# Kernel tuning notes

Measured on AMD Instinct MI355X. Metric: run time of the kernel, lower is better.

Reference implementation:

```python
import jax, jax.numpy as jnp
import numpy as np

B, T, D, U, C = 256, 512, 128, 128, 64


def setup_inputs() -> dict:
    key = jax.random.key(0)
    ks = jax.random.split(key, 4)
    s_in = 1.0 / np.sqrt(D)
    s_u = 1.0 / np.sqrt(U)
    return {
        "inputs": jax.random.normal(ks[0], (B, T, D), dtype=jnp.float32),
        "W1": jax.random.normal(ks[1], (D, U), dtype=jnp.float32) * s_in,
        "b1": jnp.zeros((U,), dtype=jnp.float32),
        "W2": jax.random.normal(ks[2], (U, U), dtype=jnp.float32) * s_u,
        "b2": jnp.zeros((U,), dtype=jnp.float32),
        "Wc": jax.random.normal(ks[3], (U, C), dtype=jnp.float32) * s_u,
        "bc": jnp.zeros((C,), dtype=jnp.float32),
    }


def reference(inputs, W1, b1, W2, b2, Wc, bc):
    # state_{t} = tanh(x_t @ W1 + b1) + tanh(state_{t-1} @ W2 + b2)
    # Input projection has no recurrent dependency -> precompute in one big GEMM.
    h = jnp.tanh(jnp.einsum("btd,du->btu", inputs, W1) + b1)  # (B, T, U)

    def step(state, h_t):
        y = h_t + jnp.tanh(state @ W2 + b2)  # (B, U)
        return y, y

    state0 = jnp.zeros((inputs.shape[0], W2.shape[0]), dtype=inputs.dtype)
    _, ys = jax.lax.scan(step, state0, jnp.swapaxes(h, 0, 1))  # ys: (T, B, U)
    features = jnp.swapaxes(ys, 0, 1)  # (B, T, U)
    # classifier: Dense head applied to stacked features
    return jnp.einsum("btu,uc->btc", features, Wc) + bc
```

## Files before the change

### kernel.cpp

```cpp
#include <hip/hip_runtime.h>

#define NB 256
#define NT 512
#define ND 128
#define NU 128
#define NC 64
#define NM (NB * NT)
#define YP 136
#define SCL 2.8853900817779268f

typedef _Float16 half2v __attribute__((ext_vector_type(2)));
typedef _Float16 half4v __attribute__((ext_vector_type(4)));
typedef _Float16 half8v __attribute__((ext_vector_type(8)));
typedef float f32x4 __attribute__((ext_vector_type(4)));
typedef float v2f __attribute__((ext_vector_type(2)));

#define MFMA(a, b, c) __builtin_amdgcn_mfma_f32_16x16x32_f16((a), (b), (c), 0, 0, 0)

__device__ __forceinline__ half2v pk2(float a, float b) {
  return __builtin_bit_cast(half2v, __builtin_amdgcn_cvt_pkrtz(a, b));
}

__device__ __forceinline__ float tanh_s(float s) {
  float e = __builtin_amdgcn_exp2f(s);
  return fmaf(-2.0f, __builtin_amdgcn_rcpf(e + 1.0f), 1.0f);
}
__device__ __forceinline__ float ym1(float s, float th) {
  float e = __builtin_amdgcn_exp2f(s);
  return fmaf(-2.0f, __builtin_amdgcn_rcpf(e + 1.0f), th);
}

__device__ __forceinline__ void wg_barrier() {
  asm volatile("s_waitcnt lgkmcnt(0)\n\ts_barrier" ::: "memory");
}

__global__ __launch_bounds__(256, 1) void k1_inproj(
    const float* __restrict__ x, const float* __restrict__ W1,
    const float* __restrict__ b1v, _Float16* __restrict__ TH)
{
  __shared__ _Float16 W1T[ND * YP];
  const int tid = (int)threadIdx.x;
  for (int i = tid; i < ND * NU / 2; i += 256) {
    int n = i & 127, kh = i >> 7;
    half2v p = {(_Float16)(SCL * W1[(size_t)(2 * kh) * NU + n]),
                (_Float16)(SCL * W1[(size_t)(2 * kh + 1) * NU + n])};
    *(half2v*)&W1T[n * YP + 2 * kh] = p;
  }
  __syncthreads();

  const int L = tid & 63, wv = tid >> 6;
  const int v = L & 15, q = L >> 4;
  const int m0 = (int)blockIdx.x * 64 + wv * 16;

  const float* xr = x + (size_t)(m0 + v) * ND + 8 * q;
  half8v xf[4];
#pragma unroll
  for (int kk = 0; kk < 4; ++kk) {
    float4 a = *(const float4*)(xr + 32 * kk);
    float4 b = *(const float4*)(xr + 32 * kk + 4);
    half2v p0 = pk2(a.x, a.y), p1 = pk2(a.z, a.w);
    half2v p2 = pk2(b.x, b.y), p3 = pk2(b.z, b.w);
    xf[kk] = (half8v){p0[0], p0[1], p1[0], p1[1], p2[0], p2[1], p3[0], p3[1]};
  }

#pragma unroll
  for (int ht = 0; ht < 8; ++ht) {
    f32x4 acc;
    {
      float4 bb = *(const float4*)&b1v[16 * ht + 4 * q];
      acc = (f32x4){SCL * bb.x, SCL * bb.y, SCL * bb.z, SCL * bb.w};
    }
#pragma unroll
    for (int kk = 0; kk < 4; ++kk) {
      half8v wa = *(const half8v*)&W1T[(16 * ht + v) * YP + 32 * kk + 8 * q];
      acc = MFMA(wa, xf[kk], acc);
    }
    half2v zlo = pk2(tanh_s(acc[0]), tanh_s(acc[1]));
    half2v zhi = pk2(tanh_s(acc[2]), tanh_s(acc[3]));
    half4v z = {zlo[0], zlo[1], zhi[0], zhi[1]};
    *(half4v*)&TH[(size_t)(m0 + v) * NU + 16 * ht + 4 * q] = z;
  }
}

__global__ __launch_bounds__(640, 1) void k2_recur(
    const _Float16* __restrict__ TH, const float* __restrict__ W2,
    const float* __restrict__ b2v, const float* __restrict__ Wc,
    const float* __restrict__ bcv, float* __restrict__ out)
{
  __shared__ _Float16 Ybuf[2][2048];

  const int tid = (int)threadIdx.x;
  const int w = tid >> 6;
  const int L = tid & 63;
  const int v = L & 15, q = L >> 4;
  const int b0 = (int)blockIdx.x * 16;
  const _Float16* rd = &Ybuf[0][0] + L * 8;
  const f32x4 zero4 = (f32x4){0.f, 0.f, 0.f, 0.f};

  if (w < 8) {
    half8v w2f[4];
#pragma unroll
    for (int kk = 0; kk < 4; ++kk) {
      half8v h;
#pragma unroll
      for (int j = 0; j < 8; ++j)
        h[j] = (_Float16)(SCL * W2[(size_t)(32 * kk + 8 * q + j) * NU + 16 * w + v]);
      w2f[kk] = h;
    }
    f32x4 racc, b2f;
    {
      const int h0 = 16 * w + 4 * q;
      float4 bb = *(const float4*)&b2v[h0];
      racc = (f32x4){SCL * bb.x, SCL * bb.y, SCL * bb.z, SCL * bb.w};
      f32x4 cs = zero4;
#pragma unroll 4
      for (int k = 0; k < NU; ++k) {
        float4 ww = *(const float4*)&W2[(size_t)k * NU + h0];
        cs += (f32x4){ww.x, ww.y, ww.z, ww.w};
      }
      b2f = racc + (f32x4){SCL * cs[0], SCL * cs[1], SCL * cs[2], SCL * cs[3]};
    }

    const _Float16* thp = TH + ((size_t)(b0 + v) * NT) * NU + 16 * w + 4 * q;
    _Float16* wr = &Ybuf[0][0] + (w >> 1) * 512 +
                   (v + 16 * (2 * (w & 1) + (q >> 1))) * 8 + 4 * (q & 1);

    half4v thr0 = *(const half4v*)(thp + 0 * NU);
    half4v thr1 = *(const half4v*)(thp + 1 * NU);
    half4v thr2 = *(const half4v*)(thp + 2 * NU);
    half4v thr3 = *(const half4v*)(thp + 3 * NU);

    __builtin_amdgcn_s_setprio(1);

#define RSTEP(T_, THR_, BUF_)                                                 \
  {                                                                           \
    half2v ylo = pk2(ym1(racc[0], (float)THR_[0]),                            \
                     ym1(racc[1], (float)THR_[1]));                           \
    half2v yhi = pk2(ym1(racc[2], (float)THR_[2]),                            \
                     ym1(racc[3], (float)THR_[3]));                           \
    half4v y4 = {ylo[0], ylo[1], yhi[0], yhi[1]};                             \
    *(half4v*)(wr + (BUF_) * 2048) = y4;                                      \
    {                                                                         \
      int tn = (T_) + 4; tn = tn < NT ? tn : NT - 1;                          \
      THR_ = *(const half4v*)(thp + (size_t)tn * NU);                         \
    }                                                                         \
    wg_barrier();                                                             \
    {                                                                         \
      half8v yf0 = *(const half8v*)(rd + (BUF_) * 2048 + 0);                  \
      half8v yf1 = *(const half8v*)(rd + (BUF_) * 2048 + 512);                \
      half8v yf2 = *(const half8v*)(rd + (BUF_) * 2048 + 1024);               \
      half8v yf3 = *(const half8v*)(rd + (BUF_) * 2048 + 1536);               \
      f32x4 ra = MFMA(w2f[0], yf0, b2f);        \
      f32x4 rb = MFMA(w2f[1], yf1, zero4);                                    \
      ra = MFMA(w2f[2], yf2, ra);                                             \
      rb = MFMA(w2f[3], yf3, rb);                                             \
      racc = ra + rb;                                                         \
    }                                                                         \
  }

#pragma unroll 1
    for (int t = 0; t < NT; t += 4) {
      RSTEP(t + 0, thr0, 0)
      RSTEP(t + 1, thr1, 1)
      RSTEP(t + 2, thr2, 0)
      RSTEP(t + 3, thr3, 1)
    }
#undef RSTEP
  } else {
    const int hw = w - 8;
    half8v wcf[2][4];
    f32x4 bcf[2];
#pragma unroll
    for (int c2 = 0; c2 < 2; ++c2) {
      const int ct = 2 * hw + c2;
#pragma unroll
      for (int kk = 0; kk < 4; ++kk) {
        half8v h;
#pragma unroll
        for (int j = 0; j < 8; ++j)
          h[j] = (_Float16)Wc[(size_t)(32 * kk + 8 * q + j) * NC + 16 * ct + v];
        wcf[c2][kk] = h;
      }
      const int c0 = 16 * ct + 4 * q;
      float4 bb = *(const float4*)&bcv[c0];
      f32x4 cs = zero4;
#pragma unroll 4
      for (int k = 0; k < NU; ++k) {
        float4 ww = *(const float4*)&Wc[(size_t)k * NC + c0];
        cs += (f32x4){ww.x, ww.y, ww.z, ww.w};
      }
      bcf[c2] = cs + (f32x4){bb.x, bb.y, bb.z, bb.w};
    }
    float* op = out + ((size_t)(b0 + v) * NT) * NC + 4 * q + 32 * hw;

    half8v pf0, pf1, pf2, pf3;
#pragma unroll 1
    for (int t = 0; t < NT; ++t) {
      wg_barrier();
      if (t > 0) {
#pragma unroll
        for (int c2 = 0; c2 < 2; ++c2) {
          f32x4 oa = MFMA(wcf[c2][0], pf0, bcf[c2]);
          f32x4 ob = MFMA(wcf[c2][1], pf1, zero4);
          oa = MFMA(wcf[c2][2], pf2, oa);
          ob = MFMA(wcf[c2][3], pf3, ob);
          f32x4 oo = oa + ob;
          *(float4*)(op + (size_t)(t - 1) * NC + 16 * c2) =
              (float4){oo[0], oo[1], oo[2], oo[3]};
        }
      }
      const _Float16* rb = rd + (t & 1) * 2048;
      pf0 = *(const half8v*)(rb + 0);
      pf1 = *(const half8v*)(rb + 512);
      pf2 = *(const half8v*)(rb + 1024);
      pf3 = *(const half8v*)(rb + 1536);
    }
    asm volatile("s_waitcnt lgkmcnt(0)" ::: "memory");
#pragma unroll
    for (int c2 = 0; c2 < 2; ++c2) {
      f32x4 oa = MFMA(wcf[c2][0], pf0, bcf[c2]);
      f32x4 ob = MFMA(wcf[c2][1], pf1, zero4);
      oa = MFMA(wcf[c2][2], pf2, oa);
      ob = MFMA(wcf[c2][3], pf3, ob);
      f32x4 oo = oa + ob;
      *(float4*)(op + (size_t)(NT - 1) * NC + 16 * c2) =
          (float4){oo[0], oo[1], oo[2], oo[3]};
    }
  }
}

__device__ __forceinline__ float fast_tanh(float x) {
  float e = __expf(2.0f * x);
  return 1.0f - 2.0f / (e + 1.0f);
}
__device__ __forceinline__ float bcast(float val, int i) {
  return __builtin_bit_cast(float, __builtin_amdgcn_readlane(__builtin_bit_cast(int, val), i));
}

__global__ __launch_bounds__(256, 1) void rnn_fallback(
    const float* __restrict__ x, const float* __restrict__ W1,
    const float* __restrict__ b1v, const float* __restrict__ W2,
    const float* __restrict__ b2v, const float* __restrict__ Wc,
    const float* __restrict__ bcv, float* __restrict__ out)
{
  __shared__ float xring[16][ND];
  __shared__ float pH[2][4][NU];
  __shared__ float pR[2][4][NU];
  __shared__ float pC[2][4][NC];

  const int tid  = (int)threadIdx.x;
  const int lane = tid & 63;
  const int kg   = tid >> 6;
  const int b    = (int)blockIdx.x;
  const float4* xr4 = (const float4*)(x + (size_t)b * NT * ND);

  v2f w1f[32], w2f[32];
  float wcf[32];
#pragma unroll
  for (int i = 0; i < 32; ++i) {
    int k = kg * 32 + i;
    w1f[i] = (v2f){W1[k * NU + lane], W1[k * NU + lane + 64]};
    w2f[i] = (v2f){W2[k * NU + lane], W2[k * NU + lane + 64]};
    wcf[i] = Wc[k * NC + lane];
  }
  const float biasc = bcv[lane];
  float bias1 = 0.f, bias2 = 0.f;
  if (lane < 32) { bias1 = b1v[kg * 32 + lane]; bias2 = b2v[kg * 32 + lane]; }

  float4 stg = make_float4(0.f, 0.f, 0.f, 0.f);
  if (lane < 32) {
    float4 a0 = xr4[(kg + 0) * 32 + lane];
    float4 a1 = xr4[(kg + 4) * 32 + lane];
    ((float4*)xring[kg + 0])[lane] = a0;
    ((float4*)xring[kg + 4])[lane] = a1;
    stg = xr4[(kg + 8) * 32 + lane];
  }
  float yseg = 0.f;
  wg_barrier();

  for (int t = 0; t < NT; ++t) {
    const int pb = t & 1;
    v2f accH0 = {0.f, 0.f}, accH1 = {0.f, 0.f};
    const float4* xb = (const float4*)&xring[t & 15][kg * 32];
#pragma unroll
    for (int i = 0; i < 4; ++i) {
      float4 xa = xb[2 * i];
      float4 xc = xb[2 * i + 1];
      accH0 = w1f[8*i+0] * (v2f){xa.x, xa.x} + accH0;
      accH1 = w1f[8*i+1] * (v2f){xa.y, xa.y} + accH1;
      accH0 = w1f[8*i+2] * (v2f){xa.z, xa.z} + accH0;
      accH1 = w1f[8*i+3] * (v2f){xa.w, xa.w} + accH1;
      accH0 = w1f[8*i+4] * (v2f){xc.x, xc.x} + accH0;
      accH1 = w1f[8*i+5] * (v2f){xc.y, xc.y} + accH1;
      accH0 = w1f[8*i+6] * (v2f){xc.z, xc.z} + accH0;
      accH1 = w1f[8*i+7] * (v2f){xc.w, xc.w} + accH1;
    }
    v2f accH = accH0 + accH1;
    v2f accR0 = {0.f, 0.f}, accR1 = {0.f, 0.f};
    float accC0 = 0.f, accC1 = 0.f;
#pragma unroll
    for (int i = 0; i < 16; ++i) {
      float s0 = bcast(yseg, 2 * i);
      float s1 = bcast(yseg, 2 * i + 1);
      accR0 = w2f[2*i+0] * (v2f){s0, s0} + accR0;
      accR1 = w2f[2*i+1] * (v2f){s1, s1} + accR1;
      accC0 = fmaf(s0, wcf[2*i+0], accC0);
      accC1 = fmaf(s1, wcf[2*i+1], accC1);
    }
    v2f accR = accR0 + accR1;
    float accC = accC0 + accC1;

    pH[pb][kg][lane]      = accH.x;
    pH[pb][kg][lane + 64] = accH.y;
    pR[pb][kg][lane]      = accR.x;
    pR[pb][kg][lane + 64] = accR.y;
    pC[pb][kg][lane]      = accC;

    if (kg == (t & 3)) {
      if (lane < 32) {
        ((float4*)xring[(t + 8) & 15])[lane] = stg;
        int r = t + 12; r = (r < NT) ? r : (NT - 1);
        stg = xr4[r * 32 + lane];
      }
    }
    wg_barrier();
    if (lane < 32) {
      const int j = kg * 32 + lane;
      float hs = bias1, rs = bias2;
#pragma unroll
      for (int g = 0; g < 4; ++g) { hs += pH[pb][g][j]; rs += pR[pb][g][j]; }
      yseg = fast_tanh(hs) + fast_tanh(rs);
    }
    if (kg == ((t + 2) & 3) && t >= 1) {
      float cs = biasc;
#pragma unroll
      for (int g = 0; g < 4; ++g) cs += pC[pb][g][lane];
      out[((size_t)b * NT + (t - 1)) * NC + lane] = cs;
    }
  }
  float accC0 = 0.f, accC1 = 0.f;
#pragma unroll
  for (int i = 0; i < 16; ++i) {
    float s0 = bcast(yseg, 2 * i);
    float s1 = bcast(yseg, 2 * i + 1);
    accC0 = fmaf(s0, wcf[2*i+0], accC0);
    accC1 = fmaf(s1, wcf[2*i+1], accC1);
  }
  pC[0][kg][lane] = accC0 + accC1;
  wg_barrier();
  if (kg == 0) {
    float cs = biasc;
#pragma unroll
    for (int g = 0; g < 4; ++g) cs += pC[0][g][lane];
    out[((size_t)b * NT + (NT - 1)) * NC + lane] = cs;
  }
}

extern "C" void kernel_launch(void* const* d_in, const int* in_sizes, int n_in,
                              void* d_out, int out_size, void* d_ws, size_t ws_size,
                              hipStream_t stream) {
  (void)in_sizes; (void)n_in; (void)out_size;
  const float* x   = (const float*)d_in[0];
  const float* W1  = (const float*)d_in[1];
  const float* b1v = (const float*)d_in[2];
  const float* W2  = (const float*)d_in[3];
  const float* b2v = (const float*)d_in[4];
  const float* Wc  = (const float*)d_in[5];
  const float* bcv = (const float*)d_in[6];
  float* out = (float*)d_out;

  const size_t need = (size_t)NM * NU * 2;
  if (ws_size >= need) {
    _Float16* TH = (_Float16*)d_ws;
    hipLaunchKernelGGL(k1_inproj, dim3(NM / 64), dim3(256), 0, stream, x, W1, b1v, TH);
    hipLaunchKernelGGL(k2_recur, dim3(NB / 16), dim3(640), 0, stream,
                       TH, W2, b2v, Wc, bcv, out);
  } else {
    hipLaunchKernelGGL(rnn_fallback, dim3(NB), dim3(256), 0, stream,
                       x, W1, b1v, W2, b2v, Wc, bcv, out);
  }
}
```

Baseline: 302.3 us.

## Fuse input projection into recurrent kernel via producer warps and LDS ring

Removes the separate input-projection kernel and its fp16 global workspace. Four extra producer waves per block compute tanh(x W1 + b1) a few timesteps ahead into an 8-slot LDS ring that the recurrent waves read each step. This drops the global round trip for TH and one kernel launch. In exchange the 16 blocks now also carry the projection GEMM, the block grows to 896 threads, and the producers join every barrier on the serial critical path. The fallback kernel is deleted.

```diff
diff --git a/kernel.cpp b/kernel.cpp
--- a/kernel.cpp
+++ b/kernel.cpp
@@ -5,15 +5,12 @@
 #define ND 128
 #define NU 128
 #define NC 64
-#define NM (NB * NT)
-#define YP 136
 #define SCL 2.8853900817779268f
 
 typedef _Float16 half2v __attribute__((ext_vector_type(2)));
 typedef _Float16 half4v __attribute__((ext_vector_type(4)));
 typedef _Float16 half8v __attribute__((ext_vector_type(8)));
 typedef float f32x4 __attribute__((ext_vector_type(4)));
-typedef float v2f __attribute__((ext_vector_type(2)));
 
 #define MFMA(a, b, c) __builtin_amdgcn_mfma_f32_16x16x32_f16((a), (b), (c), 0, 0, 0)
 
@@ -34,60 +31,14 @@
   asm volatile("s_waitcnt lgkmcnt(0)\n\ts_barrier" ::: "memory");
 }
 
-__global__ __launch_bounds__(256, 1) void k1_inproj(
+__global__ __launch_bounds__(896, 1) void rnn_fused(
     const float* __restrict__ x, const float* __restrict__ W1,
-    const float* __restrict__ b1v, _Float16* __restrict__ TH)
-{
-  __shared__ _Float16 W1T[ND * YP];
-  const int tid = (int)threadIdx.x;
-  for (int i = tid; i < ND * NU / 2; i += 256) {
-    int n = i & 127, kh = i >> 7;
-    half2v p = {(_Float16)(SCL * W1[(size_t)(2 * kh) * NU + n]),
-                (_Float16)(SCL * W1[(size_t)(2 * kh + 1) * NU + n])};
-    *(half2v*)&W1T[n * YP + 2 * kh] = p;
-  }
-  __syncthreads();
-
-  const int L = tid & 63, wv = tid >> 6;
-  const int v = L & 15, q = L >> 4;
-  const int m0 = (int)blockIdx.x * 64 + wv * 16;
-
-  const float* xr = x + (size_t)(m0 + v) * ND + 8 * q;
-  half8v xf[4];
-#pragma unroll
-  for (int kk = 0; kk < 4; ++kk) {
-    float4 a = *(const float4*)(xr + 32 * kk);
-    float4 b = *(const float4*)(xr + 32 * kk + 4);
-    half2v p0 = pk2(a.x, a.y), p1 = pk2(a.z, a.w);
-    half2v p2 = pk2(b.x, b.y), p3 = pk2(b.z, b.w);
-    xf[kk] = (half8v){p0[0], p0[1], p1[0], p1[1], p2[0], p2[1], p3[0], p3[1]};
-  }
-
-#pragma unroll
-  for (int ht = 0; ht < 8; ++ht) {
-    f32x4 acc;
-    {
-      float4 bb = *(const float4*)&b1v[16 * ht + 4 * q];
-      acc = (f32x4){SCL * bb.x, SCL * bb.y, SCL * bb.z, SCL * bb.w};
-    }
-#pragma unroll
-    for (int kk = 0; kk < 4; ++kk) {
-      half8v wa = *(const half8v*)&W1T[(16 * ht + v) * YP + 32 * kk + 8 * q];
-      acc = MFMA(wa, xf[kk], acc);
-    }
-    half2v zlo = pk2(tanh_s(acc[0]), tanh_s(acc[1]));
-    half2v zhi = pk2(tanh_s(acc[2]), tanh_s(acc[3]));
-    half4v z = {zlo[0], zlo[1], zhi[0], zhi[1]};
-    *(half4v*)&TH[(size_t)(m0 + v) * NU + 16 * ht + 4 * q] = z;
-  }
-}
-
-__global__ __launch_bounds__(640, 1) void k2_recur(
-    const _Float16* __restrict__ TH, const float* __restrict__ W2,
+    const float* __restrict__ b1v, const float* __restrict__ W2,
     const float* __restrict__ b2v, const float* __restrict__ Wc,
     const float* __restrict__ bcv, float* __restrict__ out)
 {
   __shared__ _Float16 Ybuf[2][2048];
+  __shared__ _Float16 TR[8][2048];
 
   const int tid = (int)threadIdx.x;
   const int w = tid >> 6;
@@ -120,36 +71,30 @@
       }
       b2f = racc + (f32x4){SCL * cs[0], SCL * cs[1], SCL * cs[2], SCL * cs[3]};
     }
-
-    const _Float16* thp = TH + ((size_t)(b0 + v) * NT) * NU + 16 * w + 4 * q;
     _Float16* wr = &Ybuf[0][0] + (w >> 1) * 512 +
                    (v + 16 * (2 * (w & 1) + (q >> 1))) * 8 + 4 * (q & 1);
-
-    half4v thr0 = *(const half4v*)(thp + 0 * NU);
-    half4v thr1 = *(const half4v*)(thp + 1 * NU);
-    half4v thr2 = *(const half4v*)(thp + 2 * NU);
-    half4v thr3 = *(const half4v*)(thp + 3 * NU);
+    const _Float16* trr = &TR[0][0] + w * 256 + v * 16 + q * 4;
 
     __builtin_amdgcn_s_setprio(1);
-
-#define RSTEP(T_, THR_, BUF_)                                                 \
+    wg_barrier();
+
+    half4v thr = *(const half4v*)trr;
+
+#define RSTEP(T_, BUF_)                                                       \
   {                                                                           \
-    half2v ylo = pk2(ym1(racc[0], (float)THR_[0]),                            \
-                     ym1(racc[1], (float)THR_[1]));                           \
-    half2v yhi = pk2(ym1(racc[2], (float)THR_[2]),                            \
-                     ym1(racc[3], (float)THR_[3]));                           \
+    half2v ylo = pk2(ym1(racc[0], (float)thr[0]),                             \
+                     ym1(racc[1], (float)thr[1]));                            \
+    half2v yhi = pk2(ym1(racc[2], (float)thr[2]),                             \
+                     ym1(racc[3], (float)thr[3]));                            \
     half4v y4 = {ylo[0], ylo[1], yhi[0], yhi[1]};                             \
     *(half4v*)(wr + (BUF_) * 2048) = y4;                                      \
-    {                                                                         \
-      int tn = (T_) + 4; tn = tn < NT ? tn : NT - 1;                          \
-      THR_ = *(const half4v*)(thp + (size_t)tn * NU);                         \
-    }                                                                         \
     wg_barrier();                                                             \
     {                                                                         \
       half8v yf0 = *(const half8v*)(rd + (BUF_) * 2048 + 0);                  \
       half8v yf1 = *(const half8v*)(rd + (BUF_) * 2048 + 512);                \
       half8v yf2 = *(const half8v*)(rd + (BUF_) * 2048 + 1024);               \
       half8v yf3 = *(const half8v*)(rd + (BUF_) * 2048 + 1536);               \
+      thr = *(const half4v*)(trr + (((T_) + 1) & 7) * 2048);                  \
       f32x4 ra = MFMA(w2f[0], yf0, b2f);        \
       f32x4 rb = MFMA(w2f[1], yf1, zero4);                                    \
       ra = MFMA(w2f[2], yf2, ra);                                             \
@@ -159,14 +104,13 @@
   }
 
 #pragma unroll 1
-    for (int t = 0; t < NT; t += 4) {
-      RSTEP(t + 0, thr0, 0)
-      RSTEP(t + 1, thr1, 1)
-      RSTEP(t + 2, thr2, 0)
-      RSTEP(t + 3, thr3, 1)
+    for (int t = 0; t < NT; t += 2) {
+      RSTEP(t + 0, 0)
+      RSTEP(t + 1, 1)
     }
 #undef RSTEP
-  } else {
+
+  } else if (w < 10) {
     const int hw = w - 8;
     half8v wcf[2][4];
     f32x4 bcf[2];
@@ -192,6 +136,8 @@
       bcf[c2] = cs + (f32x4){bb.x, bb.y, bb.z, bb.w};
     }
     float* op = out + ((size_t)(b0 + v) * NT) * NC + 4 * q + 32 * hw;
+
+    wg_barrier();
 
     half8v pf0, pf1, pf2, pf3;
 #pragma unroll 1
@@ -226,140 +172,86 @@
       *(float4*)(op + (size_t)(NT - 1) * NC + 16 * c2) =
           (float4){oo[0], oo[1], oo[2], oo[3]};
     }
-  }
-}
-
-__device__ __forceinline__ float fast_tanh(float x) {
-  float e = __expf(2.0f * x);
-  return 1.0f - 2.0f / (e + 1.0f);
-}
-__device__ __forceinline__ float bcast(float val, int i) {
-  return __builtin_bit_cast(float, __builtin_amdgcn_readlane(__builtin_bit_cast(int, val), i));
-}
-
-__global__ __launch_bounds__(256, 1) void rnn_fallback(
-    const float* __restrict__ x, const float* __restrict__ W1,
-    const float* __restrict__ b1v, const float* __restrict__ W2,
-    const float* __restrict__ b2v, const float* __restrict__ Wc,
-    const float* __restrict__ bcv, float* __restrict__ out)
-{
-  __shared__ float xring[16][ND];
-  __shared__ float pH[2][4][NU];
-  __shared__ float pR[2][4][NU];
-  __shared__ float pC[2][4][NC];
-
-  const int tid  = (int)threadIdx.x;
-  const int lane = tid & 63;
-  const int kg   = tid >> 6;
-  const int b    = (int)blockIdx.x;
-  const float4* xr4 = (const float4*)(x + (size_t)b * NT * ND);
-
-  v2f w1f[32], w2f[32];
-  float wcf[32];
-#pragma unroll
-  for (int i = 0; i < 32; ++i) {
-    int k = kg * 32 + i;
-    w1f[i] = (v2f){W1[k * NU + lane], W1[k * NU + lane + 64]};
-    w2f[i] = (v2f){W2[k * NU + lane], W2[k * NU + lane + 64]};
-    wcf[i] = Wc[k * NC + lane];
-  }
-  const float biasc = bcv[lane];
-  float bias1 = 0.f, bias2 = 0.f;
-  if (lane < 32) { bias1 = b1v[kg * 32 + lane]; bias2 = b2v[kg * 32 + lane]; }
-
-  float4 stg = make_float4(0.f, 0.f, 0.f, 0.f);
-  if (lane < 32) {
-    float4 a0 = xr4[(kg + 0) * 32 + lane];
-    float4 a1 = xr4[(kg + 4) * 32 + lane];
-    ((float4*)xring[kg + 0])[lane] = a0;
-    ((float4*)xring[kg + 4])[lane] = a1;
-    stg = xr4[(kg + 8) * 32 + lane];
-  }
-  float yseg = 0.f;
-  wg_barrier();
-
-  for (int t = 0; t < NT; ++t) {
-    const int pb = t & 1;
-    v2f accH0 = {0.f, 0.f}, accH1 = {0.f, 0.f};
-    const float4* xb = (const float4*)&xring[t & 15][kg * 32];
-#pragma unroll
-    for (int i = 0; i < 4; ++i) {
-      float4 xa = xb[2 * i];
-      float4 xc = xb[2 * i + 1];
-      accH0 = w1f[8*i+0] * (v2f){xa.x, xa.x} + accH0;
-      accH1 = w1f[8*i+1] * (v2f){xa.y, xa.y} + accH1;
-      accH0 = w1f[8*i+2] * (v2f){xa.z, xa.z} + accH0;
-      accH1 = w1f[8*i+3] * (v2f){xa.w, xa.w} + accH1;
-      accH0 = w1f[8*i+4] * (v2f){xc.x, xc.x} + accH0;
-      accH1 = w1f[8*i+5] * (v2f){xc.y, xc.y} + accH1;
-      accH0 = w1f[8*i+6] * (v2f){xc.z, xc.z} + accH0;
-      accH1 = w1f[8*i+7] * (v2f){xc.w, xc.w} + accH1;
-    }
-    v2f accH = accH0 + accH1;
-    v2f accR0 = {0.f, 0.f}, accR1 = {0.f, 0.f};
-    float accC0 = 0.f, accC1 = 0.f;
-#pragma unroll
-    for (int i = 0; i < 16; ++i) {
-      float s0 = bcast(yseg, 2 * i);
-      float s1 = bcast(yseg, 2 * i + 1);
-      accR0 = w2f[2*i+0] * (v2f){s0, s0} + accR0;
-      accR1 = w2f[2*i+1] * (v2f){s1, s1} + accR1;
-      accC0 = fmaf(s0, wcf[2*i+0], accC0);
-      accC1 = fmaf(s1, wcf[2*i+1], accC1);
-    }
-    v2f accR = accR0 + accR1;
-    float accC = accC0 + accC1;
-
-    pH[pb][kg][lane]      = accH.x;
-    pH[pb][kg][lane + 64] = accH.y;
-    pR[pb][kg][lane]      = accR.x;
-    pR[pb][kg][lane + 64] = accR.y;
-    pC[pb][kg][lane]      = accC;
-
-    if (kg == (t & 3)) {
-      if (lane < 32) {
-        ((float4*)xring[(t + 8) & 15])[lane] = stg;
-        int r = t + 12; r = (r < NT) ? r : (NT - 1);
-        stg = xr4[r * 32 + lane];
-      }
-    }
+
+  } else {
+    const int p = w - 10;
+    half8v w1f[2][4];
+    f32x4 b1f[2];
+#pragma unroll
+    for (int tt = 0; tt < 2; ++tt) {
+      const int ct = 2 * p + tt;
+#pragma unroll
+      for (int kk = 0; kk < 4; ++kk) {
+        half8v h;
+#pragma unroll
+        for (int j = 0; j < 8; ++j)
+          h[j] = (_Float16)(SCL * W1[(size_t)(32 * kk + 8 * q + j) * NU + 16 * ct + v]);
+        w1f[tt][kk] = h;
+      }
+      float4 bb = *(const float4*)&b1v[16 * ct + 4 * q];
+      b1f[tt] = (f32x4){SCL * bb.x, SCL * bb.y, SCL * bb.z, SCL * bb.w};
+    }
+    _Float16* trw = &TR[0][0] + v * 16 + q * 4;
+
+#define LOADX(X_, S_)                                                         \
+  {                                                                           \
+    const float* xr_ = x + ((size_t)(b0 + v) * NT + (size_t)(S_)) * ND + 8 * q;\
+    _Pragma("unroll")                                                         \
+    for (int kk = 0; kk < 4; ++kk) {                                          \
+      X_[2 * kk]     = *(const float4*)(xr_ + 32 * kk);                       \
+      X_[2 * kk + 1] = *(const float4*)(xr_ + 32 * kk + 4);                   \
+    }                                                                         \
+  }
+
+#define PRODUCE(S_, X_)                                                       \
+  {                                                                           \
+    half8v xf[4];                                                             \
+    _Pragma("unroll")                                                         \
+    for (int kk = 0; kk < 4; ++kk) {                                          \
+      float4 a = X_[2 * kk], b = X_[2 * kk + 1];                              \
+      half2v p0 = pk2(a.x, a.y), p1 = pk2(a.z, a.w);                          \
+      half2v p2 = pk2(b.x, b.y), p3 = pk2(b.z, b.w);                          \
+      xf[kk] = (half8v){p0[0], p0[1], p1[0], p1[1], p2[0], p2[1], p3[0], p3[1]};\
+    }                                                                         \
+    _Pragma("unroll")                                                         \
+    for (int tt = 0; tt < 2; ++tt) {                                          \
+      f32x4 acc = b1f[tt];                                                    \
+      _Pragma("unroll")                                                       \
+      for (int kk = 0; kk < 4; ++kk) acc = MFMA(w1f[tt][kk], xf[kk], acc);    \
+      half2v lo = pk2(tanh_s(acc[0]), tanh_s(acc[1]));                        \
+      half2v hi = pk2(tanh_s(acc[2]), tanh_s(acc[3]));                        \
+      half4v z4 = {lo[0], lo[1], hi[0], hi[1]};                               \
+      *(half4v*)(trw + ((S_) & 7) * 2048 + (2 * p + tt) * 256) = z4;          \
+    }                                                                         \
+  }
+
+    float4 X0[8], X1[8];
+    LOADX(X0, 0) LOADX(X1, 1)
+    PRODUCE(0, X0) LOADX(X0, 2)
+    PRODUCE(1, X1) LOADX(X1, 3)
+    PRODUCE(2, X0) LOADX(X0, 4)
+    PRODUCE(3, X1) LOADX(X1, 5)
+
     wg_barrier();
-    if (lane < 32) {
-      const int j = kg * 32 + lane;
-      float hs = bias1, rs = bias2;
-#pragma unroll
-      for (int g = 0; g < 4; ++g) { hs += pH[pb][g][j]; rs += pR[pb][g][j]; }
-      yseg = fast_tanh(hs) + fast_tanh(rs);
-    }
-    if (kg == ((t + 2) & 3) && t >= 1) {
-      float cs = biasc;
-#pragma unroll
-      for (int g = 0; g < 4; ++g) cs += pC[pb][g][lane];
-      out[((size_t)b * NT + (t - 1)) * NC + lane] = cs;
-    }
-  }
-  float accC0 = 0.f, accC1 = 0.f;
-#pragma unroll
-  for (int i = 0; i < 16; ++i) {
-    float s0 = bcast(yseg, 2 * i);
-    float s1 = bcast(yseg, 2 * i + 1);
-    accC0 = fmaf(s0, wcf[2*i+0], accC0);
-    accC1 = fmaf(s1, wcf[2*i+1], accC1);
-  }
-  pC[0][kg][lane] = accC0 + accC1;
-  wg_barrier();
-  if (kg == 0) {
-    float cs = biasc;
-#pragma unroll
-    for (int g = 0; g < 4; ++g) cs += pC[0][g][lane];
-    out[((size_t)b * NT + (NT - 1)) * NC + lane] = cs;
+
+#pragma unroll 1
+    for (int t = 0; t < NT; t += 2) {
+      if (t + 4 < NT) { PRODUCE(t + 4, X0) }
+      if (t + 6 < NT) { LOADX(X0, t + 6) }
+      wg_barrier();
+      if (t + 5 < NT) { PRODUCE(t + 5, X1) }
+      if (t + 7 < NT) { LOADX(X1, t + 7) }
+      wg_barrier();
+    }
+#undef PRODUCE
+#undef LOADX
   }
 }
 
 extern "C" void kernel_launch(void* const* d_in, const int* in_sizes, int n_in,
                               void* d_out, int out_size, void* d_ws, size_t ws_size,
                               hipStream_t stream) {
-  (void)in_sizes; (void)n_in; (void)out_size;
+  (void)in_sizes; (void)n_in; (void)out_size; (void)d_ws; (void)ws_size;
   const float* x   = (const float*)d_in[0];
   const float* W1  = (const float*)d_in[1];
   const float* b1v = (const float*)d_in[2];
@@ -369,14 +261,6 @@
   const float* bcv = (const float*)d_in[6];
   float* out = (float*)d_out;
 
-  const size_t need = (size_t)NM * NU * 2;
-  if (ws_size >= need) {
-    _Float16* TH = (_Float16*)d_ws;
-    hipLaunchKernelGGL(k1_inproj, dim3(NM / 64), dim3(256), 0, stream, x, W1, b1v, TH);
-    hipLaunchKernelGGL(k2_recur, dim3(NB / 16), dim3(640), 0, stream,
-                       TH, W2, b2v, Wc, bcv, out);
-  } else {
-    hipLaunchKernelGGL(rnn_fallback, dim3(NB), dim3(256), 0, stream,
-                       x, W1, b1v, W2, b2v, Wc, bcv, out);
-  }
-}
+  hipLaunchKernelGGL(rnn_fused, dim3(NB / 16), dim3(896), 0, stream,
+                     x, W1, b1v, W2, b2v, Wc, bcv, out);
+}
```

Result: slower. 571.7 us (+89.1%).
